# Performance work log

Measured on AMD Instinct MI355X. Metric: run time of the kernel, lower is better.

## Reference

```python
import jax, jax.numpy as jnp
import numpy as np
import math

D_MODEL = 1024
N_HEADS = 16
D_K = D_MODEL // N_HEADS
WIDTH_MULTIPLIER = 1.0  # readout=False on all projections, so unused in math


def setup_inputs() -> dict:
    key = jax.random.key(0)
    kx, kq, kk, kv, ko = jax.random.split(key, 5)
    std = 1.0 / math.sqrt(D_MODEL)  # init_scale=1.0 / sqrt(in_features)
    x = jax.random.normal(kx, (2, 2048, D_MODEL), dtype=jnp.float32)
    # weights stored as (out_features, in_features), matching torch
    Wq = jax.random.normal(kq, (D_MODEL, D_MODEL), dtype=jnp.float32) * std
    Wk = jax.random.normal(kk, (D_MODEL, D_MODEL), dtype=jnp.float32) * std
    Wv = jax.random.normal(kv, (D_MODEL, D_MODEL), dtype=jnp.float32) * std
    Wo = jax.random.normal(ko, (D_MODEL, D_MODEL), dtype=jnp.float32) * std
    return {"x": x, "Wq": Wq, "Wk": Wk, "Wv": Wv, "Wo": Wo}


def reference(x, Wq, Wk, Wv, Wo):
    B, S, D = x.shape
    H, Dk = N_HEADS, D_K
    # muPLinear: x @ W.T (bias=False, readout=False)
    q = jnp.einsum('bsd,ed->bse', x, Wq).reshape(B, S, H, Dk).transpose(0, 2, 1, 3)
    k = jnp.einsum('bsd,ed->bse', x, Wk).reshape(B, S, H, Dk).transpose(0, 2, 1, 3)
    v = jnp.einsum('bsd,ed->bse', x, Wv).reshape(B, S, H, Dk).transpose(0, 2, 1, 3)
    # full [B,H,S,S] scores, scaled by 1/sqrt(d_k), softmax over keys
    scores = jnp.einsum('bhqd,bhkd->bhqk', q, k) / math.sqrt(Dk)
    attn = jax.nn.softmax(scores, axis=-1)
    out = jnp.einsum('bhqk,bhkd->bhqd', attn, v)
    out = out.transpose(0, 2, 1, 3).reshape(B, S, D)
    return jnp.einsum('bsd,ed->bse', out, Wo)
```

## Files before the change

### kernel.cpp

```cpp
#include <hip/hip_runtime.h>
#include <hip/hip_bf16.h>
#include <math.h>

#define D_MODEL 1024
#define N_HEADS 16
#define D_K     64
#define BATCH   2
#define SEQ     2048
#define M_TOTAL (BATCH * SEQ)

typedef __attribute__((ext_vector_type(8))) short short8;
typedef __attribute__((ext_vector_type(2))) float f32x2;
typedef __attribute__((ext_vector_type(4))) float f32x4;
typedef __attribute__((ext_vector_type(16))) float f32x16;

__device__ __forceinline__ ushort f2bf(float f) {
    __hip_bfloat16 h = __float2bfloat16(f);
    union { __hip_bfloat16 h; ushort u; } c; c.h = h; return c.u;
}

__device__ __forceinline__ uint cvtpk(float a, float b) {
    uint r;
    asm("v_cvt_pk_bf16_f32 %0, %1, %2" : "=v"(r) : "v"(a), "v"(b));
    return r;
}

__device__ __forceinline__ f32x2 pk_mul(f32x2 a, f32x2 b) {
    f32x2 d;
    asm("v_pk_mul_f32 %0, %1, %2" : "=v"(d) : "v"(a), "v"(b));
    return d;
}
__device__ __forceinline__ f32x2 pk_add(f32x2 a, f32x2 b) {
    f32x2 d;
    asm("v_pk_add_f32 %0, %1, %2" : "=v"(d) : "v"(a), "v"(b));
    return d;
}
__device__ __forceinline__ float max3f(float a, float b, float c) {
    float d;
    asm("v_max3_f32 %0, %1, %2, %3" : "=v"(d) : "v"(a), "v"(b), "v"(c));
    return d;
}

__device__ __forceinline__ void gload_lds16(const void* g, void* l) {
    __builtin_amdgcn_global_load_lds(
        (const __attribute__((address_space(1))) void*)g,
        (__attribute__((address_space(3))) void*)l, 16, 0, 0);
}

__device__ __forceinline__ void plswap(uint& a, uint& b) {
    asm volatile("v_permlane32_swap_b32 %0, %1" : "+v"(a), "+v"(b));
}

__global__ __launch_bounds__(256) void cast_all(const float* __restrict__ x,
                                                const float* __restrict__ Wq,
                                                const float* __restrict__ Wk,
                                                const float* __restrict__ Wv,
                                                const float* __restrict__ Wo,
                                                ushort* __restrict__ xb,
                                                ushort* __restrict__ wqkv,
                                                ushort* __restrict__ wob)
{
    const int bi = blockIdx.x;
    const float* src; ushort* dst; int blk;
    const int NW = D_MODEL * D_MODEL;
    if (bi < 4096)      { src = x;  dst = xb;            blk = bi; }
    else if (bi < 5120) { src = Wq; dst = wqkv;          blk = bi - 4096; }
    else if (bi < 6144) { src = Wk; dst = wqkv + NW;     blk = bi - 5120; }
    else if (bi < 7168) { src = Wv; dst = wqkv + 2 * NW; blk = bi - 6144; }
    else                { src = Wo; dst = wob;           blk = bi - 7168; }
    const int i = blk * 1024 + threadIdx.x * 4;
    float4 v = *(const float4*)&src[i];
    ushort4 o;
    o.x = f2bf(v.x); o.y = f2bf(v.y); o.z = f2bf(v.z); o.w = f2bf(v.w);
    *(ushort4*)&dst[i] = o;
}

template <int EPI>
__global__ __launch_bounds__(256) void gemm_bf16(const ushort* __restrict__ A,
                                                 const ushort* __restrict__ B,
                                                 void* __restrict__ C0,
                                                 void* __restrict__ C1,
                                                 void* __restrict__ C2,
                                                 int M, int N, int K)
{
    __shared__ ushort As[2][4 * 128 * 8];
    __shared__ ushort Bs[2][4 * 128 * 8];

    const int tid = threadIdx.x;
    const int lane = tid & 63;
    const int w = tid >> 6;
    const int li = lane & 15;
    const int kg = lane >> 4;
    const int m0 = blockIdx.y * 128;
    const int n0 = blockIdx.x * 128;
    const int wr = (w >> 1) * 64;
    const int wc = (w & 1) * 64;

    f32x4 acc[4][4] = {};

    const int s1 = tid, s2 = tid + 256;
    const ushort* ga1 = &A[(size_t)(m0 + (s1 & 127)) * K + (s1 >> 7) * 8];
    const ushort* ga2 = &A[(size_t)(m0 + (s2 & 127)) * K + (s2 >> 7) * 8];
    const ushort* gb1 = &B[(size_t)(n0 + (s1 & 127)) * K + (s1 >> 7) * 8];
    const ushort* gb2 = &B[(size_t)(n0 + (s2 & 127)) * K + (s2 >> 7) * 8];

    const int NT = K / 32;
    gload_lds16(ga1, &As[0][s1 * 8]);
    gload_lds16(ga2, &As[0][s2 * 8]);
    gload_lds16(gb1, &Bs[0][s1 * 8]);
    gload_lds16(gb2, &Bs[0][s2 * 8]);

    for (int t = 0; t < NT; ++t) {
        const int cur = t & 1;
        asm volatile("s_waitcnt vmcnt(0)" ::: "memory");
        __syncthreads();
        if (t + 1 < NT) {
            const int kb = (t + 1) * 32;
            const int nxt = cur ^ 1;
            gload_lds16(ga1 + kb, &As[nxt][s1 * 8]);
            gload_lds16(ga2 + kb, &As[nxt][s2 * 8]);
            gload_lds16(gb1 + kb, &Bs[nxt][s1 * 8]);
            gload_lds16(gb2 + kb, &Bs[nxt][s2 * 8]);
        }
        short8 af[4], bf_[4];
#pragma unroll
        for (int m = 0; m < 4; ++m)
            af[m] = *(const short8*)&As[cur][(kg * 128 + wr + m * 16 + li) * 8];
#pragma unroll
        for (int n = 0; n < 4; ++n)
            bf_[n] = *(const short8*)&Bs[cur][(kg * 128 + wc + n * 16 + li) * 8];
#pragma unroll
        for (int m = 0; m < 4; ++m)
#pragma unroll
            for (int n = 0; n < 4; ++n)
                acc[m][n] = __builtin_amdgcn_mfma_f32_16x16x32_bf16(
                    af[m], bf_[n], acc[m][n], 0, 0, 0);
    }

    if (EPI == 1) {
        ushort* q = (ushort*)C0; ushort* k = (ushort*)C1; ushort* v = (ushort*)C2;
        const float QSCALE = 0.125f * 1.44269504088896f;
#pragma unroll
        for (int m = 0; m < 4; ++m) {
            const int Rb = m0 + wr + m * 16 + kg * 4;
#pragma unroll
            for (int n = 0; n < 4; ++n) {
                const int Ncol = n0 + wc + n * 16 + li;
                const int proj = Ncol >> 10;
                const int rem = Ncol & 1023;
                const int h = rem >> 6, dk = rem & 63;
#pragma unroll
                for (int r = 0; r < 4; ++r) {
                    const int R = Rb + r;
                    const int b = R >> 11, s = R & 2047;
                    const int bh = b * N_HEADS + h;
                    if (proj == 0)
                        q[((size_t)bh * SEQ + s) * D_K + dk] = f2bf(acc[m][n][r] * QSCALE);
                    else if (proj == 1)
                        k[((size_t)bh * SEQ + s) * D_K + dk] = f2bf(acc[m][n][r]);
                    else
                        v[((size_t)bh * D_K + dk) * SEQ + s] = f2bf(acc[m][n][r]);
                }
            }
        }
    } else {
        float* C = (float*)C0;
#pragma unroll
        for (int m = 0; m < 4; ++m) {
            const int Rb = m0 + wr + m * 16 + kg * 4;
#pragma unroll
            for (int n = 0; n < 4; ++n) {
                const int Ncol = n0 + wc + n * 16 + li;
#pragma unroll
                for (int r = 0; r < 4; ++r)
                    C[(size_t)(Rb + r) * N + Ncol] = acc[m][n][r];
            }
        }
    }
}

__global__ __launch_bounds__(512, 4) void attn_mfma(const ushort* __restrict__ Q,
                                                    const ushort* __restrict__ K,
                                                    const ushort* __restrict__ Vt,
                                                    ushort* __restrict__ AO)
{
    __shared__ ushort pool[2][2][2][64 * 64];

    const int tid = threadIdx.x, lane = tid & 63, w = tid >> 6;
    const int wq = w & 3, kvh = w >> 2;
    const int r31 = lane & 31, hi = lane >> 5;
    const int b = blockIdx.z, h = blockIdx.y, q0 = blockIdx.x * 128;
    const int bh = b * N_HEADS + h;
    const size_t base = (size_t)bh * SEQ * D_K;
    const size_t vbase = (size_t)bh * D_K * SEQ;

    uint pa = (uint)lane, pbv = 1000u + (uint)lane;
    plswap(pa, pbv);
    const bool swap_lo = (__builtin_amdgcn_readfirstlane(pa) > 500u);

    const size_t qrow = base + (size_t)(q0 + wq * 32 + r31) * D_K;
    short8 qb[4];
#pragma unroll
    for (int ks = 0; ks < 4; ++ks)
        qb[ks] = *(const short8*)&Q[qrow + ks * 16 + hi * 8];

    float m_ = -INFINITY, l_ = 0.f;
    f32x2 cpair = {0.f, 0.f};
    f32x16 o0 = {}, o1 = {};

    const int srow_l = lane >> 3;
    const int sblk = lane & 7;
    const ushort* Kt0 = &K[base];
    const ushort* Vt0 = &Vt[vbase];
    const int tile0 = kvh * 16;

    const int xr = r31 & 7;
    int off[2][4];
#pragma unroll
    for (int hf = 0; hf < 2; ++hf)
#pragma unroll
        for (int ks = 0; ks < 4; ++ks)
            off[hf][ks] = hf * 2048 + r31 * 64 + (((2 * ks + hi) ^ xr) * 8);

    const ushort* Kst = &pool[kvh][0][0][0];
    const ushort* Vst = &pool[kvh][1][0][0];

#define STAGE(kt_, buf_)                                                       \
    {                                                                          \
        _Pragma("unroll")                                                      \
        for (int p = 0; p < 2; ++p) {                                          \
            const int row = wq * 16 + p * 8 + srow_l;                          \
            const int db = sblk ^ (row & 7);                                   \
            gload_lds16(Kt0 + ((size_t)((tile0 + (kt_)) * 64 + row)) * D_K + db * 8, \
                        &pool[kvh][0][buf_][(wq * 16 + p * 8) * 64]);          \
            gload_lds16(Vt0 + (size_t)row * SEQ + (tile0 + (kt_)) * 64 + db * 8,     \
                        &pool[kvh][1][buf_][(wq * 16 + p * 8) * 64]);          \
        }                                                                      \
    }

    STAGE(0, 0);

    const int NT = SEQ / 64 / 2;
    for (int kt = 0; kt < NT; ++kt) {
        const int cur = kt & 1;
        asm volatile("s_waitcnt vmcnt(0)" ::: "memory");
        __syncthreads();
        if (kt + 1 < NT) STAGE(kt + 1, cur ^ 1);
        const int cb = cur * 4096;

        f32x16 s0 = {}, s1 = {};
        __builtin_amdgcn_s_setprio(1);
#pragma unroll
        for (int ks = 0; ks < 4; ++ks) {
            short8 kb = *(const short8*)(Kst + cb + off[0][ks]);
            s0 = __builtin_amdgcn_mfma_f32_32x32x16_bf16(kb, qb[ks], s0, 0, 0, 0);
        }
#pragma unroll
        for (int ks = 0; ks < 4; ++ks) {
            short8 kb = *(const short8*)(Kst + cb + off[1][ks]);
            s1 = __builtin_amdgcn_mfma_f32_32x32x16_bf16(kb, qb[ks], s1, 0, 0, 0);
        }
        __builtin_amdgcn_s_setprio(0);

        float t0 = max3f(s0[0], s0[1], s0[2]);
        float t1 = max3f(s0[3], s0[4], s0[5]);
        float t2 = max3f(s0[6], s0[7], s0[8]);
        float t3 = max3f(s0[9], s0[10], s0[11]);
        float t4 = max3f(s0[12], s0[13], s0[14]);
        float t5 = max3f(s0[15], s1[0], s1[1]);
        float t6 = max3f(s1[2], s1[3], s1[4]);
        float t7 = max3f(s1[5], s1[6], s1[7]);
        float t8 = max3f(s1[8], s1[9], s1[10]);
        float t9 = max3f(s1[11], s1[12], s1[13]);
        float ta = fmaxf(s1[14], s1[15]);
        t0 = max3f(t0, t1, t2);
        t3 = max3f(t3, t4, t5);
        t6 = max3f(t6, t7, t8);
        t9 = max3f(t9, ta, t0);
        float mx = max3f(t3, t6, t9);
        mx = fmaxf(mx, __shfl_xor(mx, 32, 64));

        if (__any(mx > m_ + 8.0f)) {
            const float mn = fmaxf(m_, mx);
            const float sc = exp2f(m_ - mn);
            l_ *= sc;
#pragma unroll
            for (int e = 0; e < 16; ++e) { o0[e] *= sc; o1[e] *= sc; }
            m_ = mn;
            const float c = exp2f(-m_);
            cpair.x = c; cpair.y = c;
        }

        f32x2 ts0 = {0.f, 0.f}, ts1 = {0.f, 0.f};
        uint u[8][2];
#pragma unroll
        for (int rq = 0; rq < 4; ++rq) {
            f32x2 ea = {exp2f(s0[4 * rq + 0]), exp2f(s0[4 * rq + 1])};
            f32x2 eb = {exp2f(s0[4 * rq + 2]), exp2f(s0[4 * rq + 3])};
            f32x2 pa_ = pk_mul(ea, cpair);
            f32x2 pb_ = pk_mul(eb, cpair);
            ts0 = pk_add(ts0, pa_);
            ts1 = pk_add(ts1, pb_);
            u[rq][0] = cvtpk(pa_.x, pa_.y);
            u[rq][1] = cvtpk(pb_.x, pb_.y);
        }
#pragma unroll
        for (int rq = 0; rq < 4; ++rq) {
            f32x2 ea = {exp2f(s1[4 * rq + 0]), exp2f(s1[4 * rq + 1])};
            f32x2 eb = {exp2f(s1[4 * rq + 2]), exp2f(s1[4 * rq + 3])};
            f32x2 pa_ = pk_mul(ea, cpair);
            f32x2 pb_ = pk_mul(eb, cpair);
            ts0 = pk_add(ts0, pa_);
            ts1 = pk_add(ts1, pb_);
            u[4 + rq][0] = cvtpk(pa_.x, pa_.y);
            u[4 + rq][1] = cvtpk(pb_.x, pb_.y);
        }
        f32x2 tsc = pk_add(ts0, ts1);
        float ts = tsc.x + tsc.y;
        ts += __shfl_xor(ts, 32, 64);
        l_ += ts;

        short8 pb[4];
#pragma unroll
        for (int ks = 0; ks < 4; ++ks) {
            uint x0 = u[2 * ks][0], x1 = u[2 * ks][1];
            uint y0 = u[2 * ks + 1][0], y1 = u[2 * ks + 1][1];
            if (swap_lo) { plswap(y0, x0); plswap(y1, x1); }
            else         { plswap(x0, y0); plswap(x1, y1); }
            union { uint u4[4]; short8 s; } pu;
            pu.u4[0] = x0; pu.u4[1] = x1; pu.u4[2] = y0; pu.u4[3] = y1;
            pb[ks] = pu.s;
        }

        __builtin_amdgcn_s_setprio(1);
#pragma unroll
        for (int ks = 0; ks < 4; ++ks) {
            short8 vb = *(const short8*)(Vst + cb + off[0][ks]);
            o0 = __builtin_amdgcn_mfma_f32_32x32x16_bf16(vb, pb[ks], o0, 0, 0, 0);
        }
#pragma unroll
        for (int ks = 0; ks < 4; ++ks) {
            short8 vb = *(const short8*)(Vst + cb + off[1][ks]);
            o1 = __builtin_amdgcn_mfma_f32_32x32x16_bf16(vb, pb[ks], o1, 0, 0, 0);
        }
        __builtin_amdgcn_s_setprio(0);
    }
#undef STAGE

    __syncthreads();
    float* cs = (float*)&pool[0][0][0][0];
    float* ml = cs + 4 * 64 * 32;
    const int cidx = (wq * 64 + lane) * 32;
    if (kvh == 1) {
#pragma unroll
        for (int rq = 0; rq < 4; ++rq) {
            f32x4 a, c;
#pragma unroll
            for (int e = 0; e < 4; ++e) { a[e] = o0[4 * rq + e]; c[e] = o1[4 * rq + e]; }
            *(f32x4*)&cs[cidx + 4 * rq] = a;
            *(f32x4*)&cs[cidx + 16 + 4 * rq] = c;
        }
        ml[(wq * 64 + lane) * 2]     = m_;
        ml[(wq * 64 + lane) * 2 + 1] = l_;
    }
    __syncthreads();
    if (kvh == 0) {
        const float m2 = ml[(wq * 64 + lane) * 2];
        const float l2 = ml[(wq * 64 + lane) * 2 + 1];
        const float mM = fmaxf(m_, m2);
        const float sc1 = exp2f(m_ - mM), sc2 = exp2f(m2 - mM);
        const float linv = 1.f / (l_ * sc1 + l2 * sc2);
        ushort* Ao = &AO[((size_t)b * SEQ + q0 + wq * 32 + r31) * D_MODEL + h * 64];
#pragma unroll
        for (int rq = 0; rq < 4; ++rq) {
            f32x4 a = *(const f32x4*)&cs[cidx + 4 * rq];
            f32x4 c = *(const f32x4*)&cs[cidx + 16 + 4 * rq];
            uint2 v0, v1;
            v0.x = cvtpk((o0[4 * rq + 0] * sc1 + a[0] * sc2) * linv,
                         (o0[4 * rq + 1] * sc1 + a[1] * sc2) * linv);
            v0.y = cvtpk((o0[4 * rq + 2] * sc1 + a[2] * sc2) * linv,
                         (o0[4 * rq + 3] * sc1 + a[3] * sc2) * linv);
            v1.x = cvtpk((o1[4 * rq + 0] * sc1 + c[0] * sc2) * linv,
                         (o1[4 * rq + 1] * sc1 + c[1] * sc2) * linv);
            v1.y = cvtpk((o1[4 * rq + 2] * sc1 + c[2] * sc2) * linv,
                         (o1[4 * rq + 3] * sc1 + c[3] * sc2) * linv);
            *(uint2*)&Ao[8 * rq + 4 * hi]      = v0;
            *(uint2*)&Ao[32 + 8 * rq + 4 * hi] = v1;
        }
    }
}

extern "C" void kernel_launch(void* const* d_in, const int* in_sizes, int n_in,
                              void* d_out, int out_size, void* d_ws, size_t ws_size,
                              hipStream_t stream)
{
    const float* x  = (const float*)d_in[0];
    const float* Wq = (const float*)d_in[1];
    const float* Wk = (const float*)d_in[2];
    const float* Wv = (const float*)d_in[3];
    const float* Wo = (const float*)d_in[4];
    float* out = (float*)d_out;

    ushort* xb   = (ushort*)d_ws;
    ushort* Wqkv = xb + (size_t)M_TOTAL * D_MODEL;
    ushort* Wob  = Wqkv + (size_t)3 * D_MODEL * D_MODEL;
    ushort* q    = Wob + (size_t)D_MODEL * D_MODEL;
    ushort* k    = q + (size_t)M_TOTAL * D_MODEL;
    ushort* vt   = k + (size_t)M_TOTAL * D_MODEL;
    ushort* ao   = vt + (size_t)M_TOTAL * D_MODEL;

    hipLaunchKernelGGL(cast_all, dim3(8192), dim3(256), 0, stream,
                       x, Wq, Wk, Wv, Wo, xb, Wqkv, Wob);

    hipLaunchKernelGGL((gemm_bf16<1>), dim3(3 * D_MODEL / 128, M_TOTAL / 128), dim3(256),
                       0, stream, xb, Wqkv, q, k, vt, M_TOTAL, 3 * D_MODEL, D_MODEL);

    hipLaunchKernelGGL(attn_mfma, dim3(SEQ / 128, N_HEADS, BATCH), dim3(512),
                       0, stream, q, k, vt, ao);

    hipLaunchKernelGGL((gemm_bf16<0>), dim3(D_MODEL / 128, M_TOTAL / 128), dim3(256),
                       0, stream, ao, Wob, out, (void*)0, (void*)0,
                       M_TOTAL, D_MODEL, D_MODEL);
}
```

Baseline: 171.6 us.

## Split 64-key attention tile into two 32-key halves with per-half online softmax

The inner flash-attention loop now handles each 64-key tile as two 32-key sub-tiles, running QK^T, the max/exp softmax update and the PV MFMAs once per half instead of once for the whole tile. This halves the live score and probability registers, which can lower register pressure and let the softmax of one half overlap with the MFMAs of the other. In exchange it adds a second max reduction, cross-lane shuffle and possible rescale check per tile, and the V operand reads are regrouped across the two output accumulators.

```diff
diff --git a/kernel.cpp b/kernel.cpp
--- a/kernel.cpp
+++ b/kernel.cpp
@@ -246,104 +246,79 @@
         asm volatile("s_waitcnt vmcnt(0)" ::: "memory");
         __syncthreads();
         if (kt + 1 < NT) STAGE(kt + 1, cur ^ 1);
-        const int cb = cur * 4096;
-
-        f32x16 s0 = {}, s1 = {};
-        __builtin_amdgcn_s_setprio(1);
-#pragma unroll
-        for (int ks = 0; ks < 4; ++ks) {
-            short8 kb = *(const short8*)(Kst + cb + off[0][ks]);
-            s0 = __builtin_amdgcn_mfma_f32_32x32x16_bf16(kb, qb[ks], s0, 0, 0, 0);
-        }
-#pragma unroll
-        for (int ks = 0; ks < 4; ++ks) {
-            short8 kb = *(const short8*)(Kst + cb + off[1][ks]);
-            s1 = __builtin_amdgcn_mfma_f32_32x32x16_bf16(kb, qb[ks], s1, 0, 0, 0);
-        }
-        __builtin_amdgcn_s_setprio(0);
-
-        float t0 = max3f(s0[0], s0[1], s0[2]);
-        float t1 = max3f(s0[3], s0[4], s0[5]);
-        float t2 = max3f(s0[6], s0[7], s0[8]);
-        float t3 = max3f(s0[9], s0[10], s0[11]);
-        float t4 = max3f(s0[12], s0[13], s0[14]);
-        float t5 = max3f(s0[15], s1[0], s1[1]);
-        float t6 = max3f(s1[2], s1[3], s1[4]);
-        float t7 = max3f(s1[5], s1[6], s1[7]);
-        float t8 = max3f(s1[8], s1[9], s1[10]);
-        float t9 = max3f(s1[11], s1[12], s1[13]);
-        float ta = fmaxf(s1[14], s1[15]);
-        t0 = max3f(t0, t1, t2);
-        t3 = max3f(t3, t4, t5);
-        t6 = max3f(t6, t7, t8);
-        t9 = max3f(t9, ta, t0);
-        float mx = max3f(t3, t6, t9);
-        mx = fmaxf(mx, __shfl_xor(mx, 32, 64));
-
-        if (__any(mx > m_ + 8.0f)) {
-            const float mn = fmaxf(m_, mx);
-            const float sc = exp2f(m_ - mn);
-            l_ *= sc;
-#pragma unroll
-            for (int e = 0; e < 16; ++e) { o0[e] *= sc; o1[e] *= sc; }
-            m_ = mn;
-            const float c = exp2f(-m_);
-            cpair.x = c; cpair.y = c;
-        }
-
-        f32x2 ts0 = {0.f, 0.f}, ts1 = {0.f, 0.f};
-        uint u[8][2];
-#pragma unroll
-        for (int rq = 0; rq < 4; ++rq) {
-            f32x2 ea = {exp2f(s0[4 * rq + 0]), exp2f(s0[4 * rq + 1])};
-            f32x2 eb = {exp2f(s0[4 * rq + 2]), exp2f(s0[4 * rq + 3])};
-            f32x2 pa_ = pk_mul(ea, cpair);
-            f32x2 pb_ = pk_mul(eb, cpair);
-            ts0 = pk_add(ts0, pa_);
-            ts1 = pk_add(ts1, pb_);
-            u[rq][0] = cvtpk(pa_.x, pa_.y);
-            u[rq][1] = cvtpk(pb_.x, pb_.y);
-        }
-#pragma unroll
-        for (int rq = 0; rq < 4; ++rq) {
-            f32x2 ea = {exp2f(s1[4 * rq + 0]), exp2f(s1[4 * rq + 1])};
-            f32x2 eb = {exp2f(s1[4 * rq + 2]), exp2f(s1[4 * rq + 3])};
-            f32x2 pa_ = pk_mul(ea, cpair);
-            f32x2 pb_ = pk_mul(eb, cpair);
-            ts0 = pk_add(ts0, pa_);
-            ts1 = pk_add(ts1, pb_);
-            u[4 + rq][0] = cvtpk(pa_.x, pa_.y);
-            u[4 + rq][1] = cvtpk(pb_.x, pb_.y);
-        }
-        f32x2 tsc = pk_add(ts0, ts1);
-        float ts = tsc.x + tsc.y;
-        ts += __shfl_xor(ts, 32, 64);
-        l_ += ts;
-
-        short8 pb[4];
-#pragma unroll
-        for (int ks = 0; ks < 4; ++ks) {
-            uint x0 = u[2 * ks][0], x1 = u[2 * ks][1];
-            uint y0 = u[2 * ks + 1][0], y1 = u[2 * ks + 1][1];
-            if (swap_lo) { plswap(y0, x0); plswap(y1, x1); }
-            else         { plswap(x0, y0); plswap(x1, y1); }
-            union { uint u4[4]; short8 s; } pu;
-            pu.u4[0] = x0; pu.u4[1] = x1; pu.u4[2] = y0; pu.u4[3] = y1;
-            pb[ks] = pu.s;
-        }
-
-        __builtin_amdgcn_s_setprio(1);
-#pragma unroll
-        for (int ks = 0; ks < 4; ++ks) {
-            short8 vb = *(const short8*)(Vst + cb + off[0][ks]);
-            o0 = __builtin_amdgcn_mfma_f32_32x32x16_bf16(vb, pb[ks], o0, 0, 0, 0);
-        }
-#pragma unroll
-        for (int ks = 0; ks < 4; ++ks) {
-            short8 vb = *(const short8*)(Vst + cb + off[1][ks]);
-            o1 = __builtin_amdgcn_mfma_f32_32x32x16_bf16(vb, pb[ks], o1, 0, 0, 0);
-        }
-        __builtin_amdgcn_s_setprio(0);
+        const ushort* Kc = Kst + cur * 4096;
+        const ushort* Vc = Vst + cur * 4096;
+
+#pragma unroll
+        for (int hh = 0; hh < 2; ++hh) {
+            f32x16 s = {};
+            __builtin_amdgcn_s_setprio(1);
+#pragma unroll
+            for (int ks = 0; ks < 4; ++ks) {
+                short8 kb = *(const short8*)(Kc + off[hh][ks]);
+                s = __builtin_amdgcn_mfma_f32_32x32x16_bf16(kb, qb[ks], s, 0, 0, 0);
+            }
+            __builtin_amdgcn_s_setprio(0);
+
+            float t0 = max3f(s[0], s[1], s[2]);
+            float t1 = max3f(s[3], s[4], s[5]);
+            float t2 = max3f(s[6], s[7], s[8]);
+            float t3 = max3f(s[9], s[10], s[11]);
+            float t4 = max3f(s[12], s[13], s[14]);
+            t0 = max3f(t0, t1, s[15]);
+            t2 = max3f(t2, t3, t4);
+            float mx = fmaxf(t0, t2);
+            mx = fmaxf(mx, __shfl_xor(mx, 32, 64));
+
+            if (__any(mx > m_ + 8.0f)) {
+                const float mn = fmaxf(m_, mx);
+                const float sc = exp2f(m_ - mn);
+                l_ *= sc;
+#pragma unroll
+                for (int e = 0; e < 16; ++e) { o0[e] *= sc; o1[e] *= sc; }
+                m_ = mn;
+                const float c = exp2f(-m_);
+                cpair.x = c; cpair.y = c;
+            }
+
+            f32x2 ts0 = {0.f, 0.f};
+            uint u[4][2];
+#pragma unroll
+            for (int rq = 0; rq < 4; ++rq) {
+                f32x2 ea = {exp2f(s[4 * rq + 0]), exp2f(s[4 * rq + 1])};
+                f32x2 eb = {exp2f(s[4 * rq + 2]), exp2f(s[4 * rq + 3])};
+                f32x2 pa_ = pk_mul(ea, cpair);
+                f32x2 pb_ = pk_mul(eb, cpair);
+                ts0 = pk_add(ts0, pk_add(pa_, pb_));
+                u[rq][0] = cvtpk(pa_.x, pa_.y);
+                u[rq][1] = cvtpk(pb_.x, pb_.y);
+            }
+            float ts = ts0.x + ts0.y;
+            ts += __shfl_xor(ts, 32, 64);
+            l_ += ts;
+
+            short8 pb[2];
+#pragma unroll
+            for (int ks = 0; ks < 2; ++ks) {
+                uint x0 = u[2 * ks][0], x1 = u[2 * ks][1];
+                uint y0 = u[2 * ks + 1][0], y1 = u[2 * ks + 1][1];
+                if (swap_lo) { plswap(y0, x0); plswap(y1, x1); }
+                else         { plswap(x0, y0); plswap(x1, y1); }
+                union { uint u4[4]; short8 s; } pu;
+                pu.u4[0] = x0; pu.u4[1] = x1; pu.u4[2] = y0; pu.u4[3] = y1;
+                pb[ks] = pu.s;
+            }
+
+            __builtin_amdgcn_s_setprio(1);
+#pragma unroll
+            for (int ks = 0; ks < 2; ++ks) {
+                short8 vb0 = *(const short8*)(Vc + off[0][2 * hh + ks]);
+                short8 vb1 = *(const short8*)(Vc + off[1][2 * hh + ks]);
+                o0 = __builtin_amdgcn_mfma_f32_32x32x16_bf16(vb0, pb[ks], o0, 0, 0, 0);
+                o1 = __builtin_amdgcn_mfma_f32_32x32x16_bf16(vb1, pb[ks], o1, 0, 0, 0);
+            }
+            __builtin_amdgcn_s_setprio(0);
+        }
     }
 #undef STAGE
 
```

Result: no change. 172.2 us (+0.3%).
